# Performance work log

Measured on AMD Instinct MI355X. Metric: run time of the kernel, lower is better.

## Reference

```python
import jax, jax.numpy as jnp
import numpy as np

N_FEATURES = 200
KERNEL = 50
N_WIN = N_FEATURES - KERNEL + 1  # 151 sub-vectors
HID_F = [100, 50]
HID_G = [50, 25]   # 0.5 * hidden_dims
REP = 128
BATCH = 2048
TAU = 0.01
BN_EPS = 1e-5


def _window_indices():
    start = np.arange(N_FEATURES)[:-KERNEL + 1]
    all_idx = start[:, None] + np.arange(KERNEL)                      # [N_WIN, KERNEL]
    comp = np.array([np.setdiff1d(np.arange(N_FEATURES), row) for row in all_idx])  # [N_WIN, N_FEATURES-KERNEL]
    return jnp.asarray(all_idx), jnp.asarray(comp)

ALL_IDX, COMP_IDX = _window_indices()


def setup_inputs() -> dict:
    key = jax.random.key(0)
    ks = jax.random.split(key, 8)
    def w(k, o, i):
        return jax.random.normal(k, (o, i), jnp.float32) / np.float32(np.sqrt(i))
    gd = [KERNEL] + HID_G + [REP]
    fd = [N_FEATURES - KERNEL] + HID_F + [REP]
    inp = {"x": jax.random.normal(ks[0], (BATCH, N_FEATURES), jnp.float32)}
    inp["gW0"] = w(ks[1], gd[1], gd[0])
    inp["gW1"] = w(ks[2], gd[2], gd[1])
    inp["gW2"] = w(ks[3], gd[3], gd[2])
    inp["fW0"] = w(ks[4], fd[1], fd[0])
    inp["fW1"] = w(ks[5], fd[2], fd[1])
    inp["fW2"] = w(ks[6], fd[3], fd[2])
    # torch.randperm(n_pos)[:min(max_negatives, n_pos)] with max_negatives=1000 > 151
    inp["negative_index"] = jax.random.permutation(ks[7], jnp.arange(N_WIN))
    return inp


def _bn(h):
    # BatchNorm1d on [B, C, F]: training-mode stats over (batch, feature), affine=False (bias=False)
    m = h.mean(axis=(0, 2), keepdims=True)
    v = ((h - m) ** 2).mean(axis=(0, 2), keepdims=True)
    return (h - m) * jax.lax.rsqrt(v + BN_EPS)


def _leaky(h):
    return jnp.where(h >= 0, h, 0.01 * h)


def _mlp(h, Ws, acts):
    # LinearBlock: linear (no bias) -> batchnorm -> activation, every layer incl. last
    for W, a in zip(Ws, acts):
        h = a(_bn(h @ W.T))
    return h


def _normalize_dim1(h):
    # F.normalize default dim=1 (over the window dim of [B, N_WIN, REP]), eps=1e-12
    n = jnp.sqrt((h * h).sum(axis=1, keepdims=True))
    return h / jnp.maximum(n, 1e-12)


def reference(x, gW0, gW1, gW2, fW0, fW1, fW2, negative_index):
    # positive_matrix_builder: pure gathers instead of repeat + fancy indexing
    x1 = x[:, ALL_IDX]    # [B, N_WIN, KERNEL]
    x2 = x[:, COMP_IDX]   # [B, N_WIN, N_FEATURES-KERNEL]
    pos = _normalize_dim1(_mlp(x1, [gW0, gW1, gW2], [_leaky, _leaky, _leaky]))        # enc_g
    query = _normalize_dim1(_mlp(x2, [fW0, fW1, fW2], [jnp.tanh, _leaky, _leaky]))    # enc_f
    # cal_logit
    pos_mult = (query * pos).sum(axis=-1, keepdims=True)                 # [B, N_WIN, 1]
    neg = jnp.einsum('bnd,bmd->bnm', query, pos)[:, :, negative_index]  # [B, N_WIN, N_WIN]
    mask = (jnp.eye(N_WIN, dtype=jnp.float32)[:, negative_index] == 1)[None]
    neg = jnp.where(mask, -jnp.inf, neg)
    logit = jnp.concatenate([pos_mult, neg], axis=-1) / TAU              # [B, N_WIN, 1+N_WIN]
    return jnp.transpose(logit, (0, 2, 1))                               # [B, 1+N_WIN, N_WIN]
```

## Files before the change

kernel.cpp:

```cpp
#include <hip/hip_runtime.h>
#include <math.h>
#include <string.h>

constexpr int BB   = 2048;
constexpr int NW   = 151;
constexpr int NF   = 200;
constexpr float BN_EPS = 1e-5f;

typedef __bf16 bf16x8 __attribute__((ext_vector_type(8)));
typedef float  f32x4  __attribute__((ext_vector_type(4)));
typedef unsigned short u16x8 __attribute__((ext_vector_type(8)));

__device__ __forceinline__ unsigned short f2bf(float f) {
  unsigned int u; memcpy(&u, &f, 4);
  unsigned int r = (u + 0x7FFFu + ((u >> 16) & 1u)) >> 16;
  return (unsigned short)r;
}
__device__ __forceinline__ float bf2f(unsigned short u) {
  unsigned int x = ((unsigned int)u) << 16;
  float f; memcpy(&f, &x, 4);
  return f;
}

__global__ __launch_bounds__(256) void f1scan_k(
  const float* __restrict__ x, const float* __restrict__ W,
  float* __restrict__ Df)
{
  __shared__ float Wt[150*51];
  __shared__ float xs[800];
  __shared__ float lso[3200];
  const int t  = threadIdx.x;
  const int b0 = blockIdx.x * 4;
  const int ch = blockIdx.y;
  const int bl = t >> 6;
  const int c  = t & 63;

  for (int idx = t; idx < 50*150; idx += 256) {
    int cl = idx / 150, k = idx % 150;
    Wt[k*51 + cl] = W[(ch*50 + cl)*150 + k];
  }
  for (int idx = t; idx < 800; idx += 256) {
    int b2 = idx / 200, j = idx % 200;
    xs[idx] = x[(b0 + b2)*200 + j];
  }
  __syncthreads();

  float h = 0.f;
  if (c < 50) {
    #pragma unroll 5
    for (int i = 0; i < 150; i++)
      h += Wt[i*51 + c] * xs[bl*200 + 50 + i];
  }

  for (int n0 = 0; n0 < NW; n0 += 16) {
    const int cs = (NW - n0 < 16) ? (NW - n0) : 16;
    if (c < 50) {
      for (int l = 0; l < cs; l++) {
        int n = n0 + l;
        lso[bl*800 + l*50 + c] = h;
        if (n < 150) h += Wt[n*51 + c] * (xs[bl*200 + n] - xs[bl*200 + n + 50]);
      }
    }
    __syncthreads();
    const int tot = 4*cs*50;
    for (int idx = t; idx < tot; idx += 256) {
      int b2 = idx / (cs*50), rem = idx % (cs*50);
      int l = rem / 50, cc = rem % 50;
      Df[((size_t)(b0+b2)*NW + n0 + l)*100 + ch*50 + cc] = lso[b2*800 + l*50 + cc];
    }
    __syncthreads();
  }
}

template<int C>
__global__ __launch_bounds__(256) void bnstats_k(
  const float* __restrict__ H, float* __restrict__ stats)
{
  __shared__ float red[8];
  const int n = blockIdx.x, b0 = blockIdx.y * 256, t = threadIdx.x;
  float s1 = 0.f, s2 = 0.f;
  for (int idx = t; idx < 256*C; idx += 256) {
    int b = b0 + idx / C, cc = idx % C;
    float v = H[((size_t)b*NW + n)*C + cc];
    s1 += v; s2 += v*v;
  }
  #pragma unroll
  for (int off = 32; off; off >>= 1) {
    s1 += __shfl_down(s1, off); s2 += __shfl_down(s2, off);
  }
  if ((t & 63) == 0) { red[(t>>6)*2] = s1; red[(t>>6)*2+1] = s2; }
  __syncthreads();
  if (t == 0) {
    atomicAdd(&stats[2*n],   red[0]+red[2]+red[4]+red[6]);
    atomicAdd(&stats[2*n+1], red[1]+red[3]+red[5]+red[7]);
  }
}

__global__ __launch_bounds__(256) void wcvt_k(
  const float* __restrict__ W, unsigned short* __restrict__ Wb,
  int OUT, int IN, int KP, int total)
{
  int idx = blockIdx.x*256 + threadIdx.x;
  if (idx >= total) return;
  int o = idx / KP, k = idx % KP;
  float v = (o < OUT && k < IN) ? W[o*IN + k] : 0.f;
  unsigned short hi = f2bf(v);
  float lo = v - bf2f(hi);
  Wb[idx] = hi;
  Wb[total + idx] = f2bf(lo);
}

template<int IN, int OUT, int MODE, int ACT>
__global__ __launch_bounds__(256) void layer_mfma_k(
    const float* __restrict__ X, const unsigned short* __restrict__ Wb,
    const float* __restrict__ statsPrev, float* __restrict__ H,
    float* __restrict__ statsOut)
{
  constexpr int KP   = (IN + 31) & ~31;
  constexpr int OUTP = (OUT + 15) & ~15;
  constexpr int KC   = KP / 32;
  constexpr int NT   = OUTP / 16;
  constexpr int MT   = 2;

  __shared__ float red[8];
  const int n    = blockIdx.x;
  const int b0   = blockIdx.y * 128;
  const int t    = threadIdx.x;
  const int w    = t >> 6;
  const int lane = t & 63;
  const int l16  = lane & 15;
  const int quad = lane >> 4;

  float mean = 0.f, rstd = 1.f;
  if constexpr (MODE == 2) {
    const float cnt = (float)BB * (float)IN;
    mean = statsPrev[2*n] / cnt;
    float var = statsPrev[2*n+1] / cnt - mean*mean;
    rstd = rsqrtf(var + BN_EPS);
  }

  bf16x8 af_hi[MT][KC], af_lo[MT][KC];
  #pragma unroll
  for (int mt = 0; mt < MT; mt++) {
    const int bb = b0 + (w*MT + mt)*16 + l16;
    const float* xr = (MODE == 0)
        ? (X + (size_t)bb*NF + n)
        : (X + ((size_t)bb*NW + n)*IN);
    #pragma unroll
    for (int kc = 0; kc < KC; kc++) {
      const int k0 = kc*32 + quad*8;
      float vv[8];
      if constexpr (MODE == 0) {
        #pragma unroll
        for (int j = 0; j < 8; j++) {
          int k = k0 + j;
          vv[j] = (k < IN) ? xr[k] : 0.f;
        }
      } else if constexpr (IN % 4 == 0) {
        #pragma unroll
        for (int g = 0; g < 2; g++) {
          int kg = k0 + 4*g;
          if (kg < IN) {
            float4 f = *(const float4*)(xr + kg);
            vv[4*g] = f.x; vv[4*g+1] = f.y; vv[4*g+2] = f.z; vv[4*g+3] = f.w;
          } else {
            vv[4*g] = 0.f; vv[4*g+1] = 0.f; vv[4*g+2] = 0.f; vv[4*g+3] = 0.f;
          }
        }
      } else if constexpr (IN % 2 == 0) {
        #pragma unroll
        for (int g = 0; g < 4; g++) {
          int kg = k0 + 2*g;
          if (kg < IN) {
            float2 f = *(const float2*)(xr + kg);
            vv[2*g] = f.x; vv[2*g+1] = f.y;
          } else {
            vv[2*g] = 0.f; vv[2*g+1] = 0.f;
          }
        }
      } else {
        #pragma unroll
        for (int j = 0; j < 8; j++) {
          int k = k0 + j;
          vv[j] = (k < IN) ? xr[k] : 0.f;
        }
      }
      u16x8 hi, lo;
      #pragma unroll
      for (int j = 0; j < 8; j++) {
        bool valid = (k0 + j) < IN;
        float v;
        if constexpr (MODE == 0) {
          v = vv[j];
        } else {
          float z = (vv[j] - mean) * rstd;
          float a = (ACT == 1) ? ((z >= 0.f) ? z : 0.01f*z) : tanhf(z);
          v = valid ? a : 0.f;
        }
        unsigned short h16 = f2bf(v);
        hi[j] = h16;
        lo[j] = f2bf(v - bf2f(h16));
      }
      af_hi[mt][kc] = __builtin_bit_cast(bf16x8, hi);
      af_lo[mt][kc] = __builtin_bit_cast(bf16x8, lo);
    }
  }

  float s1 = 0.f, s2 = 0.f;
  #pragma unroll
  for (int nt = 0; nt < NT; nt++) {
    const int c = nt*16 + l16;
    f32x4 acc[MT];
    #pragma unroll
    for (int mt = 0; mt < MT; mt++) acc[mt] = (f32x4){0.f, 0.f, 0.f, 0.f};
    #pragma unroll
    for (int kc = 0; kc < KC; kc++) {
      const unsigned short* wp = Wb + (size_t)(nt*16 + l16)*KP + kc*32 + quad*8;
      bf16x8 wh = *(const bf16x8*)wp;
      bf16x8 wl = *(const bf16x8*)(wp + OUTP*KP);
      #pragma unroll
      for (int mt = 0; mt < MT; mt++) {
        acc[mt] = __builtin_amdgcn_mfma_f32_16x16x32_bf16(af_hi[mt][kc], wh, acc[mt], 0, 0, 0);
        acc[mt] = __builtin_amdgcn_mfma_f32_16x16x32_bf16(af_lo[mt][kc], wh, acc[mt], 0, 0, 0);
        acc[mt] = __builtin_amdgcn_mfma_f32_16x16x32_bf16(af_hi[mt][kc], wl, acc[mt], 0, 0, 0);
      }
    }
    #pragma unroll
    for (int mt = 0; mt < MT; mt++) {
      const int mrow = (w*MT + mt)*16 + quad*4;
      #pragma unroll
      for (int r = 0; r < 4; r++) {
        float v = acc[mt][r];
        s1 += v; s2 += v*v;
        if (c < OUT)
          H[((size_t)(b0 + mrow + r)*NW + n)*OUT + c] = v;
      }
    }
  }

  #pragma unroll
  for (int off = 32; off; off >>= 1) {
    s1 += __shfl_down(s1, off); s2 += __shfl_down(s2, off);
  }
  if (lane == 0) { red[w*2] = s1; red[w*2+1] = s2; }
  __syncthreads();
  if (t == 0) {
    atomicAdd(&statsOut[2*n],   red[0]+red[2]+red[4]+red[6]);
    atomicAdd(&statsOut[2*n+1], red[1]+red[3]+red[5]+red[7]);
  }
}

__global__ __launch_bounds__(256) void normstats_k(
  const float* __restrict__ H, const float* __restrict__ stats,
  float* __restrict__ rinv)
{
  int idx = blockIdx.x*256 + threadIdx.x;
  int b = idx >> 7, d = idx & 127;
  const float cnt = (float)BB * 128.f;
  float s = 0.f;
  for (int n = 0; n < NW; n++) {
    float m = stats[2*n] / cnt;
    float var = stats[2*n+1] / cnt - m*m;
    float r = rsqrtf(var + BN_EPS);
    float v = H[((size_t)b*NW + n)*128 + d];
    float z = (v - m) * r;
    float lv = (z >= 0.f) ? z : 0.01f*z;
    s += lv*lv;
  }
  rinv[idx] = 1.f / fmaxf(sqrtf(s), 1e-12f);
}

__global__ __launch_bounds__(256) void applynorm_bf_k(
  const float* __restrict__ H, const float* __restrict__ stats,
  const float* __restrict__ rinv, unsigned int* __restrict__ Ob)
{
  size_t idx = (size_t)blockIdx.x*256 + threadIdx.x;
  int dh = (int)(idx & 63);
  size_t bn = idx >> 6;
  int n = (int)(bn % NW); int b = (int)(bn / NW);
  const float cnt = (float)BB * 128.f;
  float m = stats[2*n] / cnt;
  float var = stats[2*n+1] / cnt - m*m;
  float r = rsqrtf(var + BN_EPS);
  float2 v = *(const float2*)&H[(((size_t)b*NW + n) << 7) + 2*dh];
  float z0 = (v.x - m) * r, z1 = (v.y - m) * r;
  float l0 = (z0 >= 0.f) ? z0 : 0.01f*z0;
  float l1 = (z1 >= 0.f) ? z1 : 0.01f*z1;
  l0 *= rinv[(b << 7) + 2*dh];
  l1 *= rinv[(b << 7) + 2*dh + 1];
  unsigned int packed = (unsigned int)f2bf(l0) | ((unsigned int)f2bf(l1) << 16);
  Ob[((size_t)b*160 + n)*64 + dh] = packed;
}

__global__ void invperm_k(const int* __restrict__ perm, int* __restrict__ inv) {
  int j = threadIdx.x;
  if (j < NW) inv[perm[j]] = j;
}

__global__ __launch_bounds__(256) void final_mfma_k(
  const unsigned short* __restrict__ Qb, const unsigned short* __restrict__ Pb,
  const int* __restrict__ inv, float* __restrict__ out)
{
  __shared__ int invs[NW];
  const int b    = blockIdx.x;
  const int t    = threadIdx.x;
  const int w    = t >> 6;
  const int lane = t & 63;
  const int l16  = lane & 15;
  const int quad = lane >> 4;
  for (int i = t; i < NW; i += 256) invs[i] = inv[i];
  __syncthreads();

  const __bf16* Qp = (const __bf16*)(Qb + (size_t)b*160*128);
  const __bf16* Pp = (const __bf16*)(Pb + (size_t)b*160*128);
  float* ob = out + (size_t)b*152*NW;
  const float NEG_BIG = -3.0e38f;

  for (int ti = w; ti < 10; ti += 4) {
    const int mbase = ti*16;
    bf16x8 af[4];
    #pragma unroll
    for (int kc = 0; kc < 4; kc++)
      af[kc] = *(const bf16x8*)(Pp + (mbase + l16)*128 + kc*32 + quad*8);
    for (int tj = 0; tj < 10; tj++) {
      const int nbase = tj*16;
      f32x4 acc = {0.f, 0.f, 0.f, 0.f};
      #pragma unroll
      for (int kc = 0; kc < 4; kc++) {
        bf16x8 bf = *(const bf16x8*)(Qp + (nbase + l16)*128 + kc*32 + quad*8);
        acc = __builtin_amdgcn_mfma_f32_16x16x32_bf16(af[kc], bf, acc, 0, 0, 0);
      }
      const int n = nbase + l16;
      if (n < NW) {
        #pragma unroll
        for (int r = 0; r < 4; r++) {
          const int m = mbase + quad*4 + r;
          if (m < NW) {
            float v = acc[r] * 100.f;
            int orow = 1 + invs[m];
            if (m == n) {
              ob[(size_t)orow*NW + n] = NEG_BIG;
              ob[n] = v;
            } else {
              ob[(size_t)orow*NW + n] = v;
            }
          }
        }
      }
    }
  }
}

extern "C" void kernel_launch(void* const* d_in, const int* in_sizes, int n_in,
                              void* d_out, int out_size, void* d_ws, size_t ws_size,
                              hipStream_t stream) {
  const float* x   = (const float*)d_in[0];
  const float* gW0 = (const float*)d_in[1];
  const float* gW1 = (const float*)d_in[2];
  const float* gW2 = (const float*)d_in[3];
  const float* fW0 = (const float*)d_in[4];
  const float* fW1 = (const float*)d_in[5];
  const float* fW2 = (const float*)d_in[6];
  const int*  perm = (const int*)d_in[7];
  float* out = (float*)d_out;
  char* ws = (char*)d_ws;

  float* stats = (float*)ws;
  int*   inv   = (int*)(ws + 8192);
  float* rinvP = (float*)(ws + 16384);
  float* rinvQ = rinvP + 2048*128;
  float* Ag = (float*)(ws + 16384 + 2*1048576);
  float* Bg = Ag + 15462400;
  float* Cg = Bg + 7731200;
  float* Df = Cg + 39583744;
  float* Ff = Df + 30924800;
  float* Ef = Ag;
  unsigned short* Qb = (unsigned short*)Ag;
  unsigned short* Pb = (unsigned short*)Df;

  unsigned short* Wbase = (unsigned short*)(ws + 16384);
  unsigned short* Wg1 = Wbase;
  unsigned short* Wg2 = Wbase + 8192;
  unsigned short* Wg3 = Wbase + 12288;
  unsigned short* Wf2 = Wbase + 20480;
  unsigned short* Wf3 = Wbase + 36864;

  float* sg1 = stats,        *sg2 = stats + 302,  *sg3 = stats + 604;
  float* sf1 = stats + 906,  *sf2 = stats + 1208, *sf3 = stats + 1510;

  hipMemsetAsync(stats, 0, 1812*sizeof(float), stream);
  invperm_k<<<1, 192, 0, stream>>>(perm, inv);

  wcvt_k<<<16, 256, 0, stream>>>(gW0, Wg1,  50,  50,  64, 4096);
  wcvt_k<<< 8, 256, 0, stream>>>(gW1, Wg2,  25,  50,  64, 2048);
  wcvt_k<<<16, 256, 0, stream>>>(gW2, Wg3, 128,  25,  32, 4096);
  wcvt_k<<<32, 256, 0, stream>>>(fW1, Wf2,  50, 100, 128, 8192);
  wcvt_k<<<32, 256, 0, stream>>>(fW2, Wf3, 128,  50,  64, 8192);

  f1scan_k<<<dim3(BB/4, 2), 256, 0, stream>>>(x, fW0, Df);
  bnstats_k<100><<<dim3(NW, 8), 256, 0, stream>>>(Df, sf1);

  dim3 gl2(NW, BB/128);
  layer_mfma_k< 50,  50, 0, 0><<<gl2, 256, 0, stream>>>(x,  Wg1, nullptr, Ag, sg1);
  layer_mfma_k< 50,  25, 2, 1><<<gl2, 256, 0, stream>>>(Ag, Wg2, sg1,     Bg, sg2);
  layer_mfma_k< 25, 128, 2, 1><<<gl2, 256, 0, stream>>>(Bg, Wg3, sg2,     Cg, sg3);
  layer_mfma_k<100,  50, 2, 2><<<gl2, 256, 0, stream>>>(Df, Wf2, sf1,     Ef, sf2);
  layer_mfma_k< 50, 128, 2, 1><<<gl2, 256, 0, stream>>>(Ef, Wf3, sf2,     Ff, sf3);

  normstats_k  <<<1024,  256, 0, stream>>>(Cg, sg3, rinvP);
  applynorm_bf_k<<<77312, 256, 0, stream>>>(Cg, sg3, rinvP, (unsigned int*)Pb);
  normstats_k  <<<1024,  256, 0, stream>>>(Ff, sf3, rinvQ);
  applynorm_bf_k<<<77312, 256, 0, stream>>>(Ff, sf3, rinvQ, (unsigned int*)Qb);

  final_mfma_k<<<BB, 256, 0, stream>>>(Qb, Pb, inv, out);
  (void)in_sizes; (void)n_in; (void)out_size; (void)ws_size;
}
```

Baseline: 992.2 us.

## Fuse BN/normalize/bf16 conversion into final MFMA kernel with LDS staging

Removes the two applynorm kernels. The final kernel now reads the fp32 encoder outputs directly, applies BN, leaky ReLU and the L2 scaling, and packs the results into swizzled bf16 tiles in LDS. MFMA operands are then loaded from LDS instead of global memory. Results go through a per-wave LDS staging buffer so each output row is written with coalesced stores. This saves a bf16 round trip through global memory, but uses about 120KB of LDS per block, which limits occupancy to one block per CU.

```diff
diff --git a/kernel.cpp b/kernel.cpp
--- a/kernel.cpp
+++ b/kernel.cpp
@@ -270,82 +270,114 @@
   rinv[idx] = 1.f / fmaxf(sqrtf(s), 1e-12f);
 }
 
-__global__ __launch_bounds__(256) void applynorm_bf_k(
-  const float* __restrict__ H, const float* __restrict__ stats,
-  const float* __restrict__ rinv, unsigned int* __restrict__ Ob)
-{
-  size_t idx = (size_t)blockIdx.x*256 + threadIdx.x;
-  int dh = (int)(idx & 63);
-  size_t bn = idx >> 6;
-  int n = (int)(bn % NW); int b = (int)(bn / NW);
-  const float cnt = (float)BB * 128.f;
-  float m = stats[2*n] / cnt;
-  float var = stats[2*n+1] / cnt - m*m;
-  float r = rsqrtf(var + BN_EPS);
-  float2 v = *(const float2*)&H[(((size_t)b*NW + n) << 7) + 2*dh];
-  float z0 = (v.x - m) * r, z1 = (v.y - m) * r;
-  float l0 = (z0 >= 0.f) ? z0 : 0.01f*z0;
-  float l1 = (z1 >= 0.f) ? z1 : 0.01f*z1;
-  l0 *= rinv[(b << 7) + 2*dh];
-  l1 *= rinv[(b << 7) + 2*dh + 1];
-  unsigned int packed = (unsigned int)f2bf(l0) | ((unsigned int)f2bf(l1) << 16);
-  Ob[((size_t)b*160 + n)*64 + dh] = packed;
-}
-
 __global__ void invperm_k(const int* __restrict__ perm, int* __restrict__ inv) {
   int j = threadIdx.x;
   if (j < NW) inv[perm[j]] = j;
 }
 
-__global__ __launch_bounds__(256) void final_mfma_k(
-  const unsigned short* __restrict__ Qb, const unsigned short* __restrict__ Pb,
+__global__ __launch_bounds__(256) void fusedfinal_k(
+  const float* __restrict__ P32, const float* __restrict__ Q32,
+  const float* __restrict__ sP, const float* __restrict__ sQ,
+  const float* __restrict__ rinvP, const float* __restrict__ rinvQ,
   const int* __restrict__ inv, float* __restrict__ out)
 {
+  __shared__ unsigned short Pl[160*128];
+  __shared__ unsigned short Ql[160*128];
+  __shared__ float stgbuf[4][16*161];
   __shared__ int invs[NW];
+
   const int b    = blockIdx.x;
   const int t    = threadIdx.x;
   const int w    = t >> 6;
   const int lane = t & 63;
   const int l16  = lane & 15;
   const int quad = lane >> 4;
+  const float cnt = (float)BB * 128.f;
+
   for (int i = t; i < NW; i += 256) invs[i] = inv[i];
+
+  for (int idx = t; idx < 9*32; idx += 256) {
+    int row = 151 + idx/32, l = idx%32;
+    unsigned int off = (unsigned int)(row*256 + l*8) ^ (unsigned int)((row&7)<<4);
+    *(uint2*)((char*)Pl + off) = make_uint2(0u, 0u);
+    *(uint2*)((char*)Ql + off) = make_uint2(0u, 0u);
+  }
+
+  {
+    const int l32 = t & 31;
+    const int r8  = t >> 5;
+    const int d0  = l32*4;
+    const float4 riP = *(const float4*)&rinvP[(b<<7) + d0];
+    const float4 riQ = *(const float4*)&rinvQ[(b<<7) + d0];
+    for (int n = r8; n < NW; n += 8) {
+      float mP = sP[2*n] / cnt;
+      float vP = sP[2*n+1] / cnt - mP*mP;
+      float rP = rsqrtf(vP + BN_EPS);
+      float4 v = *(const float4*)&P32[((size_t)b*NW + n)*128 + d0];
+      float z0=(v.x-mP)*rP, z1=(v.y-mP)*rP, z2=(v.z-mP)*rP, z3=(v.w-mP)*rP;
+      z0 = ((z0>=0.f)?z0:0.01f*z0) * riP.x;
+      z1 = ((z1>=0.f)?z1:0.01f*z1) * riP.y;
+      z2 = ((z2>=0.f)?z2:0.01f*z2) * riP.z;
+      z3 = ((z3>=0.f)?z3:0.01f*z3) * riP.w;
+      unsigned int p0 = (unsigned int)f2bf(z0) | ((unsigned int)f2bf(z1) << 16);
+      unsigned int p1 = (unsigned int)f2bf(z2) | ((unsigned int)f2bf(z3) << 16);
+      unsigned int off = (unsigned int)(n*256 + d0*2) ^ (unsigned int)((n&7)<<4);
+      *(uint2*)((char*)Pl + off) = make_uint2(p0, p1);
+
+      float mQ = sQ[2*n] / cnt;
+      float vQ = sQ[2*n+1] / cnt - mQ*mQ;
+      float rQ = rsqrtf(vQ + BN_EPS);
+      float4 u = *(const float4*)&Q32[((size_t)b*NW + n)*128 + d0];
+      float y0=(u.x-mQ)*rQ, y1=(u.y-mQ)*rQ, y2=(u.z-mQ)*rQ, y3=(u.w-mQ)*rQ;
+      y0 = ((y0>=0.f)?y0:0.01f*y0) * riQ.x;
+      y1 = ((y1>=0.f)?y1:0.01f*y1) * riQ.y;
+      y2 = ((y2>=0.f)?y2:0.01f*y2) * riQ.z;
+      y3 = ((y3>=0.f)?y3:0.01f*y3) * riQ.w;
+      unsigned int q0 = (unsigned int)f2bf(y0) | ((unsigned int)f2bf(y1) << 16);
+      unsigned int q1 = (unsigned int)f2bf(y2) | ((unsigned int)f2bf(y3) << 16);
+      *(uint2*)((char*)Ql + off) = make_uint2(q0, q1);
+    }
+  }
   __syncthreads();
 
-  const __bf16* Qp = (const __bf16*)(Qb + (size_t)b*160*128);
-  const __bf16* Pp = (const __bf16*)(Pb + (size_t)b*160*128);
   float* ob = out + (size_t)b*152*NW;
+  float* stg = stgbuf[w];
   const float NEG_BIG = -3.0e38f;
 
   for (int ti = w; ti < 10; ti += 4) {
     const int mbase = ti*16;
     bf16x8 af[4];
     #pragma unroll
-    for (int kc = 0; kc < 4; kc++)
-      af[kc] = *(const bf16x8*)(Pp + (mbase + l16)*128 + kc*32 + quad*8);
+    for (int kc = 0; kc < 4; kc++) {
+      int row = mbase + l16;
+      unsigned int off = (unsigned int)(row*256 + (kc*32+quad*8)*2)
+                       ^ (unsigned int)((row&7)<<4);
+      af[kc] = *(const bf16x8*)((const char*)Pl + off);
+    }
+    #pragma unroll 2
     for (int tj = 0; tj < 10; tj++) {
-      const int nbase = tj*16;
       f32x4 acc = {0.f, 0.f, 0.f, 0.f};
       #pragma unroll
       for (int kc = 0; kc < 4; kc++) {
-        bf16x8 bf = *(const bf16x8*)(Qp + (nbase + l16)*128 + kc*32 + quad*8);
+        int row = tj*16 + l16;
+        unsigned int off = (unsigned int)(row*256 + (kc*32+quad*8)*2)
+                         ^ (unsigned int)((row&7)<<4);
+        bf16x8 bf = *(const bf16x8*)((const char*)Ql + off);
         acc = __builtin_amdgcn_mfma_f32_16x16x32_bf16(af[kc], bf, acc, 0, 0, 0);
       }
-      const int n = nbase + l16;
-      if (n < NW) {
-        #pragma unroll
-        for (int r = 0; r < 4; r++) {
-          const int m = mbase + quad*4 + r;
-          if (m < NW) {
-            float v = acc[r] * 100.f;
-            int orow = 1 + invs[m];
-            if (m == n) {
-              ob[(size_t)orow*NW + n] = NEG_BIG;
-              ob[n] = v;
-            } else {
-              ob[(size_t)orow*NW + n] = v;
-            }
-          }
-        }
+      #pragma unroll
+      for (int r = 0; r < 4; r++)
+        stg[(quad*4 + r)*161 + tj*16 + l16] = acc[r];
+    }
+    for (int r = 0; r < 16; r++) {
+      const int mm = mbase + r;
+      if (mm >= NW) break;
+      const int orow = 1 + invs[mm];
+      float* dst = ob + (size_t)orow*NW;
+      for (int col = lane; col < NW; col += 64) {
+        float v = stg[r*161 + col] * 100.f;
+        if (col == mm) { ob[mm] = v; v = NEG_BIG; }
+        dst[col] = v;
       }
     }
   }
@@ -375,8 +407,6 @@
   float* Df = Cg + 39583744;
   float* Ff = Df + 30924800;
   float* Ef = Ag;
-  unsigned short* Qb = (unsigned short*)Ag;
-  unsigned short* Pb = (unsigned short*)Df;
 
   unsigned short* Wbase = (unsigned short*)(ws + 16384);
   unsigned short* Wg1 = Wbase;
@@ -407,11 +437,9 @@
   layer_mfma_k<100,  50, 2, 2><<<gl2, 256, 0, stream>>>(Df, Wf2, sf1,     Ef, sf2);
   layer_mfma_k< 50, 128, 2, 1><<<gl2, 256, 0, stream>>>(Ef, Wf3, sf2,     Ff, sf3);
 
-  normstats_k  <<<1024,  256, 0, stream>>>(Cg, sg3, rinvP);
-  applynorm_bf_k<<<77312, 256, 0, stream>>>(Cg, sg3, rinvP, (unsigned int*)Pb);
-  normstats_k  <<<1024,  256, 0, stream>>>(Ff, sf3, rinvQ);
-  applynorm_bf_k<<<77312, 256, 0, stream>>>(Ff, sf3, rinvQ, (unsigned int*)Qb);
-
-  final_mfma_k<<<BB, 256, 0, stream>>>(Qb, Pb, inv, out);
+  normstats_k<<<1024, 256, 0, stream>>>(Cg, sg3, rinvP);
+  normstats_k<<<1024, 256, 0, stream>>>(Ff, sf3, rinvQ);
+
+  fusedfinal_k<<<BB, 256, 0, stream>>>(Cg, Ff, sg3, sf3, rinvP, rinvQ, inv, out);
   (void)in_sizes; (void)n_in; (void)out_size; (void)ws_size;
 }
```

New measurement: 944.7 us. 4.8% less time.
